# Kernel optimization log

Measured on AMD Instinct MI355X. Metric: run time of the kernel, lower is better.

The kernel has to match this reference:

```python
import jax, jax.numpy as jnp
import numpy as np

EPS = 1e-5


def _bn(h, gamma, beta):
    # BatchNorm1d in training mode: batch statistics over node dim
    mu = h.mean(axis=0)
    var = h.var(axis=0)
    return gamma * (h - mu) * jax.lax.rsqrt(var + EPS) + beta


def _rgcn_layer(x, src, dst, etype, W, Wloop, b, n_dst):
    # Relation-specific gather-transform-scatter (DGL RelGraphConv, sum agg,
    # self-loop + bias, no regularizer).
    x_src = x[src]                                   # [E, in] gather
    num_rels = W.shape[0]
    m = jnp.zeros((x_src.shape[0], W.shape[2]), x.dtype)
    for r in range(num_rels):                        # small fixed relation count
        m = m + jnp.where((etype == r)[:, None], x_src @ W[r], 0.0)
    agg = jax.ops.segment_sum(m, dst, num_segments=n_dst)  # scatter-add to dst
    # DGL block convention: dst nodes are the prefix of src nodes
    return agg + x[:n_dst] @ Wloop + b


def setup_inputs() -> dict:
    key = jax.random.key(0)
    ks = jax.random.split(key, 16)
    N_SRC, N_DST0, N_DST1 = 200000, 50000, 10000
    E0, E1, R, H, C = 800000, 160000, 5, 256, 153
    s = 1.0 / np.sqrt(H)
    inp = {
        "x": jax.random.normal(ks[0], (N_SRC, H), jnp.float32),
        "src0": jax.random.randint(ks[1], (E0,), 0, N_SRC, jnp.int32),
        "dst0": jax.random.randint(ks[2], (E0,), 0, N_DST0, jnp.int32),
        "etype0": jax.random.randint(ks[3], (E0,), 0, R, jnp.int32),
        "src1": jax.random.randint(ks[4], (E1,), 0, N_DST0, jnp.int32),
        "dst1": jax.random.randint(ks[5], (E1,), 0, N_DST1, jnp.int32),
        "etype1": jax.random.randint(ks[6], (E1,), 0, R, jnp.int32),
        "n_dst0": N_DST0,
        "n_dst1": N_DST1,
        "W0": jax.random.normal(ks[7], (R, H, H), jnp.float32) * s,
        "Wl0": jax.random.normal(ks[8], (H, H), jnp.float32) * s,
        "b0": jnp.zeros((H,), jnp.float32),
        "g0": jnp.ones((H,), jnp.float32),
        "be0": jnp.zeros((H,), jnp.float32),
        "W1": jax.random.normal(ks[9], (R, H, H), jnp.float32) * s,
        "Wl1": jax.random.normal(ks[10], (H, H), jnp.float32) * s,
        "b1": jnp.zeros((H,), jnp.float32),
        "g1": jnp.ones((H,), jnp.float32),
        "be1": jnp.zeros((H,), jnp.float32),
        "Wm1": jax.random.normal(ks[11], (H, H), jnp.float32) * s,
        "bm1": jnp.zeros((H,), jnp.float32),
        "gm": jnp.ones((H,), jnp.float32),
        "bem": jnp.zeros((H,), jnp.float32),
        "Wm2": jax.random.normal(ks[12], (H, C), jnp.float32) * s,
        "bm2": jnp.zeros((C,), jnp.float32),
    }
    return inp


def reference(x, src0, dst0, etype0, src1, dst1, etype1, n_dst0, n_dst1,
              W0, Wl0, b0, g0, be0, W1, Wl1, b1, g1, be1,
              Wm1, bm1, gm, bem, Wm2, bm2):
    # layer 0
    h = _rgcn_layer(x, src0, dst0, etype0, W0, Wl0, b0, n_dst0)
    h = jax.nn.elu(_bn(h, g0, be0))
    # layer 1
    h = _rgcn_layer(h, src1, dst1, etype1, W1, Wl1, b1, n_dst1)
    h = jax.nn.elu(_bn(h, g1, be1))
    # MLP head (dropout is identity in eval)
    h = jax.nn.relu(_bn(h @ Wm1 + bm1, gm, bem))
    return h @ Wm2 + bm2
```

## Files before the change

kernel.cpp:

```cpp
#include <hip/hip_runtime.h>
#include <hip/hip_bf16.h>


#define HD   256
#define EPS  1e-5f
#define NREL 5
#define ND0  50000
#define ND1  10000

typedef unsigned short ushort_t;
using f32x4  = __attribute__((ext_vector_type(4))) float;
using short8 = __attribute__((ext_vector_type(8))) short;

__device__ __forceinline__ ushort_t f2b(float f) {
    union { float f; unsigned u; } x; x.f = f;
    unsigned r = x.u + 0x7FFF + ((x.u >> 16) & 1);
    return (ushort_t)(r >> 16);
}
__device__ __forceinline__ float b2f(ushort_t h) {
    union { unsigned u; float f; } x; x.u = ((unsigned)h) << 16;
    return x.f;
}

#define GLOAD_LDS16(gp, lp)                                                     \
    __builtin_amdgcn_global_load_lds(                                           \
        (const __attribute__((address_space(1))) unsigned int*)(gp),            \
        (__attribute__((address_space(3))) unsigned int*)(lp), 16, 0, 0)

struct WconvArgs {
    const float* src[14];
    ushort_t*    dst[14];
    int          N[14];
};
__global__ void wconv_all_kernel(WconvArgs a) {
    int mat = blockIdx.x >> 8;
    int id = (blockIdx.x & 255) * 256 + threadIdx.x;
    int n = id >> 8, k = id & 255;
    int N = a.N[mat];
    float v = (n < N) ? a.src[mat][(size_t)k * N + n] : 0.f;
    a.dst[mat][id] = f2b(v);
}

__global__ void xconv_kernel(const float* __restrict__ x, ushort_t* __restrict__ xb,
                             int n4) {
    int id = blockIdx.x * 256 + threadIdx.x;
    if (id >= n4) return;
    float4 v = ((const float4*)x)[id];
    ushort4 o; o.x = f2b(v.x); o.y = f2b(v.y); o.z = f2b(v.z); o.w = f2b(v.w);
    ((ushort4*)xb)[id] = o;
}

__global__ void count2_kernel(const int* __restrict__ d0, const int* __restrict__ e0, int E0,
                              const int* __restrict__ d1, const int* __restrict__ e1, int E1,
                              int* __restrict__ cnt, int* __restrict__ pos) {
    int e = blockIdx.x * 256 + threadIdx.x;
    if (e < E0) {
        pos[e] = atomicAdd(&cnt[e0[e] * ND0 + d0[e]], 1);
    } else if (e < E0 + E1) {
        int i = e - E0;
        pos[e] = atomicAdd(&cnt[NREL * ND0 + e1[i] * ND1 + d1[i]], 1);
    }
}

__global__ void scan_block_kernel(const int* __restrict__ in, int* __restrict__ out,
                                  int* __restrict__ bsum, int nb) {
    __shared__ int ts[256];
    int tid = threadIdx.x;
    int base = blockIdx.x * 1024 + tid * 4;
    int v0 = (base + 0 < nb) ? in[base + 0] : 0;
    int v1 = (base + 1 < nb) ? in[base + 1] : 0;
    int v2 = (base + 2 < nb) ? in[base + 2] : 0;
    int v3 = (base + 3 < nb) ? in[base + 3] : 0;
    int tsum = v0 + v1 + v2 + v3;
    ts[tid] = tsum;
    __syncthreads();
    for (int d = 1; d < 256; d <<= 1) {
        int t = (tid >= d) ? ts[tid - d] : 0;
        __syncthreads();
        ts[tid] += t;
        __syncthreads();
    }
    int excl = ts[tid] - tsum;
    if (base + 0 < nb) out[base + 0] = excl;
    if (base + 1 < nb) out[base + 1] = excl + v0;
    if (base + 2 < nb) out[base + 2] = excl + v0 + v1;
    if (base + 3 < nb) out[base + 3] = excl + v0 + v1 + v2;
    if (tid == 255 && bsum) bsum[blockIdx.x] = ts[255];
}

__global__ void scan_add_kernel(int* __restrict__ out, const int* __restrict__ bsum, int nb) {
    int i = blockIdx.x * 256 + threadIdx.x;
    if (i < nb) out[i] += bsum[i >> 10];
}

__global__ void fill2_kernel(const int* __restrict__ s0, const int* __restrict__ d0,
                             const int* __restrict__ e0, int E0,
                             const int* __restrict__ s1, const int* __restrict__ d1,
                             const int* __restrict__ e1, int E1,
                             const int* __restrict__ pos, const int* __restrict__ off,
                             int* __restrict__ ssrc) {
    int e = blockIdx.x * 256 + threadIdx.x;
    if (e < E0) {
        ssrc[off[e0[e] * ND0 + d0[e]] + pos[e]] = s0[e];
    } else if (e < E0 + E1) {
        int i = e - E0;
        ssrc[off[NREL * ND0 + e1[i] * ND1 + d1[i]] + pos[e]] = s1[i];
    }
}

__device__ __forceinline__ void bnelu_acc(ushort4 v, const float4& scv, const float4& shv,
                                          float& a0, float& a1, float& a2, float& a3) {
    float f0 = fmaf(b2f(v.x), scv.x, shv.x);
    float f1 = fmaf(b2f(v.y), scv.y, shv.y);
    float f2 = fmaf(b2f(v.z), scv.z, shv.z);
    float f3 = fmaf(b2f(v.w), scv.w, shv.w);
    a0 += f0 > 0.f ? f0 : expm1f(f0);
    a1 += f1 > 0.f ? f1 : expm1f(f1);
    a2 += f2 > 0.f ? f2 : expm1f(f2);
    a3 += f3 > 0.f ? f3 : expm1f(f3);
}

__global__ void gather_kernel(const ushort_t* __restrict__ feat, const int* __restrict__ ssrc,
                              const int* __restrict__ cnt, const int* __restrict__ off,
                              int nbuckets, ushort_t* __restrict__ out,
                              const float* __restrict__ sc, const float* __restrict__ sh) {
    int wave = (blockIdx.x * 256 + threadIdx.x) >> 6;
    int lane = threadIdx.x & 63;
    if (wave >= nbuckets) return;
    int deg = cnt[wave], s = off[wave];
    float a0 = 0, a1 = 0, a2 = 0, a3 = 0;
    if (sc) {
        float4 scv = ((const float4*)sc)[lane];
        float4 shv = ((const float4*)sh)[lane];
        int j = 0;
        for (; j + 4 <= deg; j += 4) {
            int r0 = ssrc[s + j + 0], r1 = ssrc[s + j + 1];
            int r2 = ssrc[s + j + 2], r3 = ssrc[s + j + 3];
            ushort4 v0 = ((const ushort4*)(feat + (size_t)r0 * HD))[lane];
            ushort4 v1 = ((const ushort4*)(feat + (size_t)r1 * HD))[lane];
            ushort4 v2 = ((const ushort4*)(feat + (size_t)r2 * HD))[lane];
            ushort4 v3 = ((const ushort4*)(feat + (size_t)r3 * HD))[lane];
            bnelu_acc(v0, scv, shv, a0, a1, a2, a3);
            bnelu_acc(v1, scv, shv, a0, a1, a2, a3);
            bnelu_acc(v2, scv, shv, a0, a1, a2, a3);
            bnelu_acc(v3, scv, shv, a0, a1, a2, a3);
        }
        for (; j < deg; j++) {
            ushort4 v = ((const ushort4*)(feat + (size_t)ssrc[s + j] * HD))[lane];
            bnelu_acc(v, scv, shv, a0, a1, a2, a3);
        }
    } else {
        int j = 0;
        for (; j + 4 <= deg; j += 4) {
            int r0 = ssrc[s + j + 0], r1 = ssrc[s + j + 1];
            int r2 = ssrc[s + j + 2], r3 = ssrc[s + j + 3];
            ushort4 v0 = ((const ushort4*)(feat + (size_t)r0 * HD))[lane];
            ushort4 v1 = ((const ushort4*)(feat + (size_t)r1 * HD))[lane];
            ushort4 v2 = ((const ushort4*)(feat + (size_t)r2 * HD))[lane];
            ushort4 v3 = ((const ushort4*)(feat + (size_t)r3 * HD))[lane];
            a0 += b2f(v0.x) + b2f(v1.x) + b2f(v2.x) + b2f(v3.x);
            a1 += b2f(v0.y) + b2f(v1.y) + b2f(v2.y) + b2f(v3.y);
            a2 += b2f(v0.z) + b2f(v1.z) + b2f(v2.z) + b2f(v3.z);
            a3 += b2f(v0.w) + b2f(v1.w) + b2f(v2.w) + b2f(v3.w);
        }
        for (; j < deg; j++) {
            ushort4 v = ((const ushort4*)(feat + (size_t)ssrc[s + j] * HD))[lane];
            a0 += b2f(v.x); a1 += b2f(v.y); a2 += b2f(v.z); a3 += b2f(v.w);
        }
    }
    ushort4 o; o.x = f2b(a0); o.y = f2b(a1); o.z = f2b(a2); o.w = f2b(a3);
    ((ushort4*)(out + (size_t)wave * HD))[lane] = o;
}

__global__ void bnprep_kernel(const float* __restrict__ sums, const float* __restrict__ g,
                              const float* __restrict__ be, float invM,
                              float* __restrict__ sc, float* __restrict__ sh) {
    int c = threadIdx.x;
    float mu = sums[c] * invM;
    float var = sums[HD + c] * invM - mu * mu;
    float s = g[c] * rsqrtf(var + EPS);
    sc[c] = s; sh[c] = be[c] - mu * s;
}

struct Seg {
    const ushort_t* A;
    const ushort_t* B;
    const float* sc;
    const float* sh;
    int act;
};
struct GemmArgs {
    Seg seg[6];
    int nseg;
    const float* bias;
    float* stats;
    ushort_t* Cb;
    float* Cf;
    int M, N;
};

template <int BM>
__launch_bounds__(256, 4)
__global__ void gemm_mfma_kernel(GemmArgs g) {
    constexpr int F   = BM / 32;
    constexpr int NFT = BM / 16;
    constexpr int IT  = NFT / 4;
    __shared__ __align__(1024) ushort_t As[2][NFT * 512];
    __shared__ __align__(1024) ushort_t Bs[2][NFT * 512];
    int tid = threadIdx.x;
    int wave = tid >> 6, lane = tid & 63;
    int rq = lane >> 4, ci = lane & 15;
    int wm = (wave >> 1) * (BM / 2), wn = (wave & 1) * (BM / 2);
    int wmf = wm >> 4, wnf = wn >> 4;
    int bm = blockIdx.y * BM, bn = blockIdx.x * BM;
    f32x4 acc[F][F] = {};
    int K = g.nseg * HD;
    int NT = K >> 5;

    auto stage = [&](int b, int t) {
        int k = t << 5;
        int si = k >> 8;
        int kl = k & 255;
        const ushort_t* Ap = g.seg[si].A;
        const ushort_t* Bp = g.seg[si].B;
        const float* sc = g.seg[si].sc;
        if (!sc) {
#pragma unroll
            for (int it = 0; it < IT; it++) {
                int mt = it * 4 + wave;
                GLOAD_LDS16(Ap + (size_t)(bm + mt * 16 + ci) * HD + kl + rq * 8,
                            &As[b][mt * 512 + lane * 8]);
            }
        } else {
            const float* sh = g.seg[si].sh;
            int act = g.seg[si].act;
            int kb = kl + rq * 8;
#pragma unroll
            for (int it = 0; it < IT; it++) {
                int mt = it * 4 + wave;
                uint4 v = *(const uint4*)(Ap + (size_t)(bm + mt * 16 + ci) * HD + kb);
                ushort_t* u = (ushort_t*)&v;
#pragma unroll
                for (int jj = 0; jj < 8; jj++) {
                    float fv = fmaf(b2f(u[jj]), sc[kb + jj], sh[kb + jj]);
                    fv = (act == 2) ? fmaxf(fv, 0.f) : (fv > 0.f ? fv : expm1f(fv));
                    u[jj] = f2b(fv);
                }
                *(uint4*)&As[b][mt * 512 + lane * 8] = v;
            }
        }
#pragma unroll
        for (int it = 0; it < IT; it++) {
            int nt = it * 4 + wave;
            GLOAD_LDS16(Bp + (size_t)(bn + nt * 16 + ci) * HD + kl + rq * 8,
                        &Bs[b][nt * 512 + lane * 8]);
        }
    };

    stage(0, 0);
    __syncthreads();
    for (int t = 0; t < NT; t++) {
        int cur = t & 1;
        if (t + 1 < NT) stage(cur ^ 1, t + 1);
        short8 a[F], b[F];
#pragma unroll
        for (int mi = 0; mi < F; mi++)
            a[mi] = *(const short8*)&As[cur][(wmf + mi) * 512 + lane * 8];
#pragma unroll
        for (int ni = 0; ni < F; ni++)
            b[ni] = *(const short8*)&Bs[cur][(wnf + ni) * 512 + lane * 8];
#pragma unroll
        for (int mi = 0; mi < F; mi++)
#pragma unroll
            for (int ni = 0; ni < F; ni++)
                acc[mi][ni] = __builtin_amdgcn_mfma_f32_16x16x32_bf16(
                    a[mi], b[ni], acc[mi][ni], 0, 0, 0);
        __syncthreads();
    }

#pragma unroll
    for (int ni = 0; ni < F; ni++) {
        int col = bn + wn + ni * 16 + ci;
        float bv = (col < g.N) ? g.bias[col] : 0.f;
#pragma unroll
        for (int mi = 0; mi < F; mi++)
#pragma unroll
            for (int reg = 0; reg < 4; reg++) acc[mi][ni][reg] += bv;
    }
    if (g.stats) {
#pragma unroll
        for (int ni = 0; ni < F; ni++) {
            float s = 0.f, s2 = 0.f;
#pragma unroll
            for (int mi = 0; mi < F; mi++)
#pragma unroll
                for (int reg = 0; reg < 4; reg++) {
                    int row = bm + wm + mi * 16 + rq * 4 + reg;
                    if (row < g.M) { float v = acc[mi][ni][reg]; s += v; s2 += v * v; }
                }
            s  += __shfl_xor(s, 16);  s  += __shfl_xor(s, 32);
            s2 += __shfl_xor(s2, 16); s2 += __shfl_xor(s2, 32);
            if (rq == 0) {
                int col = bn + wn + ni * 16 + ci;
                atomicAdd(&g.stats[col], s);
                atomicAdd(&g.stats[HD + col], s2);
            }
        }
    }
#pragma unroll
    for (int mi = 0; mi < F; mi++)
#pragma unroll
        for (int ni = 0; ni < F; ni++)
#pragma unroll
            for (int reg = 0; reg < 4; reg++) {
                int row = bm + wm + mi * 16 + rq * 4 + reg;
                int col = bn + wn + ni * 16 + ci;
                if (row < g.M && col < g.N) {
                    float v = acc[mi][ni][reg];
                    if (g.Cb) g.Cb[(size_t)row * HD + col] = f2b(v);
                    else      g.Cf[(size_t)row * g.N + col] = v;
                }
            }
}

extern "C" void kernel_launch(void* const* d_in, const int* in_sizes, int n_in,
                              void* d_out, int out_size, void* d_ws, size_t ws_size,
                              hipStream_t stream) {
    const float* x   = (const float*)d_in[0];
    const int* src0  = (const int*)d_in[1];
    const int* dst0  = (const int*)d_in[2];
    const int* et0   = (const int*)d_in[3];
    const int* src1  = (const int*)d_in[4];
    const int* dst1  = (const int*)d_in[5];
    const int* et1   = (const int*)d_in[6];
    const float* W0  = (const float*)d_in[9];
    const float* Wl0 = (const float*)d_in[10];
    const float* b0  = (const float*)d_in[11];
    const float* g0  = (const float*)d_in[12];
    const float* be0 = (const float*)d_in[13];
    const float* W1  = (const float*)d_in[14];
    const float* Wl1 = (const float*)d_in[15];
    const float* b1  = (const float*)d_in[16];
    const float* g1  = (const float*)d_in[17];
    const float* be1 = (const float*)d_in[18];
    const float* Wm1 = (const float*)d_in[19];
    const float* bm1 = (const float*)d_in[20];
    const float* gm  = (const float*)d_in[21];
    const float* bem = (const float*)d_in[22];
    const float* Wm2 = (const float*)d_in[23];
    const float* bm2 = (const float*)d_in[24];

    const int E0 = in_sizes[1];
    const int E1 = in_sizes[4];
    const int NOUT = in_sizes[24];
    const int NSRC = in_sizes[0] / HD;
    const int NBKT = NREL * ND0 + NREL * ND1;

    char* p = (char*)d_ws;
    ushort_t* Wt = (ushort_t*)p;  p += (size_t)14 * 65536 * 2;
    float* st    = (float*)p;     p += 1536 * 4;
    float* bnp   = (float*)p;     p += 6 * 256 * 4;
    int* cnt     = (int*)p;       p += (size_t)NBKT * 4;
    int* off     = (int*)p;       p += (size_t)NBKT * 4;
    int* bsum    = (int*)p;       p += 1024 * 4;
    int* pos     = (int*)p;       p += (size_t)(E0 + E1) * 4;
    int* ssrc    = (int*)p;       p += (size_t)(E0 + E1) * 4;
    ushort_t* xb  = (ushort_t*)p; p += (size_t)NSRC * HD * 2;
    ushort_t* S0  = (ushort_t*)p; p += (size_t)(NREL * ND0 + 128) * HD * 2;
    ushort_t* S1  = (ushort_t*)p; p += (size_t)(NREL * ND1 + 128) * HD * 2;
    ushort_t* h0b = (ushort_t*)p; p += (size_t)(ND0 + 128) * HD * 2;
    ushort_t* h1b = (ushort_t*)p; p += (size_t)(ND1 + 128) * HD * 2;
    ushort_t* mb  = (ushort_t*)p; p += (size_t)(ND1 + 128) * HD * 2;

    float* st0 = st, *st1 = st + 512, *stm = st + 1024;
    float* sc0 = bnp, *sh0 = bnp + 256, *sc1 = bnp + 512, *sh1 = bnp + 768;
    float* scm = bnp + 1024, *shm = bnp + 1280;

    ushort_t* W0t  = Wt;
    ushort_t* Wl0t = Wt + 5 * 65536;
    ushort_t* W1t  = Wt + 6 * 65536;
    ushort_t* Wl1t = Wt + 11 * 65536;
    ushort_t* Wm1t = Wt + 12 * 65536;
    ushort_t* Wm2t = Wt + 13 * 65536;

    {
        WconvArgs wa;
        for (int r = 0; r < NREL; r++) { wa.src[r] = W0 + (size_t)r * 65536; wa.dst[r] = W0t + (size_t)r * 65536; wa.N[r] = 256; }
        wa.src[5] = Wl0; wa.dst[5] = Wl0t; wa.N[5] = 256;
        for (int r = 0; r < NREL; r++) { wa.src[6 + r] = W1 + (size_t)r * 65536; wa.dst[6 + r] = W1t + (size_t)r * 65536; wa.N[6 + r] = 256; }
        wa.src[11] = Wl1; wa.dst[11] = Wl1t; wa.N[11] = 256;
        wa.src[12] = Wm1; wa.dst[12] = Wm1t; wa.N[12] = 256;
        wa.src[13] = Wm2; wa.dst[13] = Wm2t; wa.N[13] = NOUT;
        wconv_all_kernel<<<14 * 256, 256, 0, stream>>>(wa);
    }
    xconv_kernel<<<(NSRC * 64 + 255) / 256, 256, 0, stream>>>(x, xb, NSRC * 64);
    hipMemsetAsync(st, 0, 1536 * sizeof(float), stream);
    hipMemsetAsync(cnt, 0, (size_t)NBKT * sizeof(int), stream);

    int ET = E0 + E1;
    count2_kernel<<<(ET + 255) / 256, 256, 0, stream>>>(dst0, et0, E0, dst1, et1, E1, cnt, pos);
    int nsb = (NBKT + 1023) / 1024;
    scan_block_kernel<<<nsb, 256, 0, stream>>>(cnt, off, bsum, NBKT);
    scan_block_kernel<<<1, 256, 0, stream>>>(bsum, bsum, nullptr, nsb);
    scan_add_kernel<<<(NBKT + 255) / 256, 256, 0, stream>>>(off, bsum, NBKT);
    fill2_kernel<<<(ET + 255) / 256, 256, 0, stream>>>(src0, dst0, et0, E0, src1, dst1, et1, E1, pos, off, ssrc);

    gather_kernel<<<(NREL * ND0 * 64) / 256, 256, 0, stream>>>(
        xb, ssrc, cnt, off, NREL * ND0, S0, nullptr, nullptr);
    {
        GemmArgs ga = {};
        for (int s = 0; s < NREL; s++)
            ga.seg[s] = { S0 + (size_t)s * ND0 * HD, W0t + (size_t)s * 65536, nullptr, nullptr, 0 };
        ga.seg[5] = { xb, Wl0t, nullptr, nullptr, 0 };
        ga.nseg = 6; ga.bias = b0; ga.stats = st0;
        ga.Cb = h0b; ga.Cf = nullptr; ga.M = ND0; ga.N = HD;
        gemm_mfma_kernel<128><<<dim3(2, (ND0 + 127) / 128), 256, 0, stream>>>(ga);
    }
    bnprep_kernel<<<1, 256, 0, stream>>>(st0, g0, be0, 1.f / ND0, sc0, sh0);

    gather_kernel<<<(NREL * ND1 * 64) / 256, 256, 0, stream>>>(
        h0b, ssrc, cnt + NREL * ND0, off + NREL * ND0, NREL * ND1, S1, sc0, sh0);
    {
        GemmArgs ga = {};
        for (int s = 0; s < NREL; s++)
            ga.seg[s] = { S1 + (size_t)s * ND1 * HD, W1t + (size_t)s * 65536, nullptr, nullptr, 0 };
        ga.seg[5] = { h0b, Wl1t, sc0, sh0, 1 };
        ga.nseg = 6; ga.bias = b1; ga.stats = st1;
        ga.Cb = h1b; ga.Cf = nullptr; ga.M = ND1; ga.N = HD;
        gemm_mfma_kernel<64><<<dim3(4, (ND1 + 63) / 64), 256, 0, stream>>>(ga);
    }
    bnprep_kernel<<<1, 256, 0, stream>>>(st1, g1, be1, 1.f / ND1, sc1, sh1);

    {
        GemmArgs ga = {};
        ga.seg[0] = { h1b, Wm1t, sc1, sh1, 1 };
        ga.nseg = 1; ga.bias = bm1; ga.stats = stm;
        ga.Cb = mb; ga.Cf = nullptr; ga.M = ND1; ga.N = HD;
        gemm_mfma_kernel<64><<<dim3(4, (ND1 + 63) / 64), 256, 0, stream>>>(ga);
    }
    bnprep_kernel<<<1, 256, 0, stream>>>(stm, gm, bem, 1.f / ND1, scm, shm);
    {
        GemmArgs ga = {};
        ga.seg[0] = { mb, Wm2t, scm, shm, 2 };
        ga.nseg = 1; ga.bias = bm2; ga.stats = nullptr;
        ga.Cb = nullptr; ga.Cf = (float*)d_out; ga.M = ND1; ga.N = NOUT;
        gemm_mfma_kernel<64><<<dim3((NOUT + 63) / 64, (ND1 + 63) / 64), 256, 0, stream>>>(ga);
    }
}
```

Measured before the change: 774.4 us.

## Use 256x256 tile GEMM with 4-stage pipeline and separate BN-activation pass

Replaces the templated 2-stage GEMM with a single 512-thread kernel that computes a full 256-column tile per block. It uses a 4-deep LDS ring with explicit vmcnt waits and one barrier per k-step. The BN+activation that was fused into the A-operand load is moved into standalone bnact kernels that write activated bf16 copies, so every GEMM can use direct global-to-LDS loads. This trades extra elementwise passes and buffers for larger reuse and deeper prefetch. It also raises LDS use and pushes the 153-column output GEMM through a 256-wide tile.

Result: slower. 808.4 us (+4.4%).

```diff
diff --git a/kernel.cpp b/kernel.cpp
--- a/kernel.cpp
+++ b/kernel.cpp
@@ -182,12 +182,35 @@
     sc[c] = s; sh[c] = be[c] - mu * s;
 }
 
+__global__ void bnact_kernel(const ushort_t* __restrict__ in, ushort_t* __restrict__ out,
+                             const float* __restrict__ sc, const float* __restrict__ sh,
+                             int act, int n64) {
+    int id = blockIdx.x * 256 + threadIdx.x;
+    if (id >= n64) return;
+    int c4 = id & 63;
+    ushort4 v = ((const ushort4*)in)[id];
+    float4 scv = ((const float4*)sc)[c4];
+    float4 shv = ((const float4*)sh)[c4];
+    float f0 = fmaf(b2f(v.x), scv.x, shv.x);
+    float f1 = fmaf(b2f(v.y), scv.y, shv.y);
+    float f2 = fmaf(b2f(v.z), scv.z, shv.z);
+    float f3 = fmaf(b2f(v.w), scv.w, shv.w);
+    if (act == 2) {
+        f0 = fmaxf(f0, 0.f); f1 = fmaxf(f1, 0.f);
+        f2 = fmaxf(f2, 0.f); f3 = fmaxf(f3, 0.f);
+    } else {
+        f0 = f0 > 0.f ? f0 : expm1f(f0);
+        f1 = f1 > 0.f ? f1 : expm1f(f1);
+        f2 = f2 > 0.f ? f2 : expm1f(f2);
+        f3 = f3 > 0.f ? f3 : expm1f(f3);
+    }
+    ushort4 o; o.x = f2b(f0); o.y = f2b(f1); o.z = f2b(f2); o.w = f2b(f3);
+    ((ushort4*)out)[id] = o;
+}
+
 struct Seg {
     const ushort_t* A;
     const ushort_t* B;
-    const float* sc;
-    const float* sh;
-    int act;
 };
 struct GemmArgs {
     Seg seg[6];
@@ -199,100 +222,74 @@
     int M, N;
 };
 
-template <int BM>
-__launch_bounds__(256, 4)
-__global__ void gemm_mfma_kernel(GemmArgs g) {
-    constexpr int F   = BM / 32;
-    constexpr int NFT = BM / 16;
-    constexpr int IT  = NFT / 4;
-    __shared__ __align__(1024) ushort_t As[2][NFT * 512];
-    __shared__ __align__(1024) ushort_t Bs[2][NFT * 512];
+__launch_bounds__(512, 2)
+__global__ void gemm256_kernel(GemmArgs g) {
+    __shared__ __align__(1024) ushort_t As[4][8192];
+    __shared__ __align__(1024) ushort_t Bs[4][8192];
     int tid = threadIdx.x;
-    int wave = tid >> 6, lane = tid & 63;
+    int w = tid >> 6, lane = tid & 63;
     int rq = lane >> 4, ci = lane & 15;
-    int wm = (wave >> 1) * (BM / 2), wn = (wave & 1) * (BM / 2);
-    int wmf = wm >> 4, wnf = wn >> 4;
-    int bm = blockIdx.y * BM, bn = blockIdx.x * BM;
-    f32x4 acc[F][F] = {};
-    int K = g.nseg * HD;
-    int NT = K >> 5;
+    int wm = (w >> 2) * 128, wn = (w & 3) * 64;
+    int bm = blockIdx.y * 256;
+    f32x4 acc[8][4] = {};
+    int NT = (g.nseg * HD) >> 5;
 
     auto stage = [&](int b, int t) {
         int k = t << 5;
-        int si = k >> 8;
-        int kl = k & 255;
+        int si = k >> 8, kl = k & 255;
         const ushort_t* Ap = g.seg[si].A;
         const ushort_t* Bp = g.seg[si].B;
-        const float* sc = g.seg[si].sc;
-        if (!sc) {
-#pragma unroll
-            for (int it = 0; it < IT; it++) {
-                int mt = it * 4 + wave;
-                GLOAD_LDS16(Ap + (size_t)(bm + mt * 16 + ci) * HD + kl + rq * 8,
-                            &As[b][mt * 512 + lane * 8]);
-            }
-        } else {
-            const float* sh = g.seg[si].sh;
-            int act = g.seg[si].act;
-            int kb = kl + rq * 8;
-#pragma unroll
-            for (int it = 0; it < IT; it++) {
-                int mt = it * 4 + wave;
-                uint4 v = *(const uint4*)(Ap + (size_t)(bm + mt * 16 + ci) * HD + kb);
-                ushort_t* u = (ushort_t*)&v;
-#pragma unroll
-                for (int jj = 0; jj < 8; jj++) {
-                    float fv = fmaf(b2f(u[jj]), sc[kb + jj], sh[kb + jj]);
-                    fv = (act == 2) ? fmaxf(fv, 0.f) : (fv > 0.f ? fv : expm1f(fv));
-                    u[jj] = f2b(fv);
-                }
-                *(uint4*)&As[b][mt * 512 + lane * 8] = v;
-            }
-        }
-#pragma unroll
-        for (int it = 0; it < IT; it++) {
-            int nt = it * 4 + wave;
-            GLOAD_LDS16(Bp + (size_t)(bn + nt * 16 + ci) * HD + kl + rq * 8,
-                        &Bs[b][nt * 512 + lane * 8]);
-        }
+        int ft = w * 2;
+        GLOAD_LDS16(Ap + (size_t)(bm + ft * 16 + ci) * HD + kl + rq * 8,
+                    &As[b][ft * 512 + lane * 8]);
+        GLOAD_LDS16(Ap + (size_t)(bm + ft * 16 + 16 + ci) * HD + kl + rq * 8,
+                    &As[b][(ft + 1) * 512 + lane * 8]);
+        GLOAD_LDS16(Bp + (size_t)(ft * 16 + ci) * HD + kl + rq * 8,
+                    &Bs[b][ft * 512 + lane * 8]);
+        GLOAD_LDS16(Bp + (size_t)(ft * 16 + 16 + ci) * HD + kl + rq * 8,
+                    &Bs[b][(ft + 1) * 512 + lane * 8]);
     };
 
     stage(0, 0);
-    __syncthreads();
+    if (NT > 1) stage(1, 1);
+    if (NT > 2) stage(2, 2);
     for (int t = 0; t < NT; t++) {
-        int cur = t & 1;
-        if (t + 1 < NT) stage(cur ^ 1, t + 1);
-        short8 a[F], b[F];
-#pragma unroll
-        for (int mi = 0; mi < F; mi++)
-            a[mi] = *(const short8*)&As[cur][(wmf + mi) * 512 + lane * 8];
-#pragma unroll
-        for (int ni = 0; ni < F; ni++)
-            b[ni] = *(const short8*)&Bs[cur][(wnf + ni) * 512 + lane * 8];
-#pragma unroll
-        for (int mi = 0; mi < F; mi++)
-#pragma unroll
-            for (int ni = 0; ni < F; ni++)
+        int buf = t & 3;
+        int rem = NT - t;
+        if (rem >= 3)      asm volatile("s_waitcnt vmcnt(8)" ::: "memory");
+        else if (rem == 2) asm volatile("s_waitcnt vmcnt(4)" ::: "memory");
+        else               asm volatile("s_waitcnt vmcnt(0)" ::: "memory");
+        __builtin_amdgcn_s_barrier();
+        if (t + 3 < NT) stage((t + 3) & 3, t + 3);
+        short8 bfr[4];
+#pragma unroll
+        for (int ni = 0; ni < 4; ni++)
+            bfr[ni] = *(const short8*)&Bs[buf][((wn >> 4) + ni) * 512 + lane * 8];
+#pragma unroll
+        for (int mi = 0; mi < 8; mi++) {
+            short8 afr = *(const short8*)&As[buf][((wm >> 4) + mi) * 512 + lane * 8];
+#pragma unroll
+            for (int ni = 0; ni < 4; ni++)
                 acc[mi][ni] = __builtin_amdgcn_mfma_f32_16x16x32_bf16(
-                    a[mi], b[ni], acc[mi][ni], 0, 0, 0);
-        __syncthreads();
-    }
-
-#pragma unroll
-    for (int ni = 0; ni < F; ni++) {
-        int col = bn + wn + ni * 16 + ci;
+                    afr, bfr[ni], acc[mi][ni], 0, 0, 0);
+        }
+    }
+
+#pragma unroll
+    for (int ni = 0; ni < 4; ni++) {
+        int col = wn + ni * 16 + ci;
         float bv = (col < g.N) ? g.bias[col] : 0.f;
 #pragma unroll
-        for (int mi = 0; mi < F; mi++)
+        for (int mi = 0; mi < 8; mi++)
 #pragma unroll
             for (int reg = 0; reg < 4; reg++) acc[mi][ni][reg] += bv;
     }
     if (g.stats) {
 #pragma unroll
-        for (int ni = 0; ni < F; ni++) {
+        for (int ni = 0; ni < 4; ni++) {
             float s = 0.f, s2 = 0.f;
 #pragma unroll
-            for (int mi = 0; mi < F; mi++)
+            for (int mi = 0; mi < 8; mi++)
 #pragma unroll
                 for (int reg = 0; reg < 4; reg++) {
                     int row = bm + wm + mi * 16 + rq * 4 + reg;
@@ -301,20 +298,20 @@
             s  += __shfl_xor(s, 16);  s  += __shfl_xor(s, 32);
             s2 += __shfl_xor(s2, 16); s2 += __shfl_xor(s2, 32);
             if (rq == 0) {
-                int col = bn + wn + ni * 16 + ci;
+                int col = wn + ni * 16 + ci;
                 atomicAdd(&g.stats[col], s);
                 atomicAdd(&g.stats[HD + col], s2);
             }
         }
     }
 #pragma unroll
-    for (int mi = 0; mi < F; mi++)
-#pragma unroll
-        for (int ni = 0; ni < F; ni++)
+    for (int mi = 0; mi < 8; mi++)
+#pragma unroll
+        for (int ni = 0; ni < 4; ni++)
 #pragma unroll
             for (int reg = 0; reg < 4; reg++) {
                 int row = bm + wm + mi * 16 + rq * 4 + reg;
-                int col = bn + wn + ni * 16 + ci;
+                int col = wn + ni * 16 + ci;
                 if (row < g.M && col < g.N) {
                     float v = acc[mi][ni][reg];
                     if (g.Cb) g.Cb[(size_t)row * HD + col] = f2b(v);
@@ -366,11 +363,14 @@
     int* pos     = (int*)p;       p += (size_t)(E0 + E1) * 4;
     int* ssrc    = (int*)p;       p += (size_t)(E0 + E1) * 4;
     ushort_t* xb  = (ushort_t*)p; p += (size_t)NSRC * HD * 2;
-    ushort_t* S0  = (ushort_t*)p; p += (size_t)(NREL * ND0 + 128) * HD * 2;
-    ushort_t* S1  = (ushort_t*)p; p += (size_t)(NREL * ND1 + 128) * HD * 2;
-    ushort_t* h0b = (ushort_t*)p; p += (size_t)(ND0 + 128) * HD * 2;
-    ushort_t* h1b = (ushort_t*)p; p += (size_t)(ND1 + 128) * HD * 2;
-    ushort_t* mb  = (ushort_t*)p; p += (size_t)(ND1 + 128) * HD * 2;
+    ushort_t* S0  = (ushort_t*)p; p += (size_t)(NREL * ND0 + 512) * HD * 2;
+    ushort_t* S1  = (ushort_t*)p; p += (size_t)(NREL * ND1 + 512) * HD * 2;
+    ushort_t* h0b = (ushort_t*)p; p += (size_t)(ND0 + 512) * HD * 2;
+    ushort_t* h1b = (ushort_t*)p; p += (size_t)(ND1 + 512) * HD * 2;
+    ushort_t* mb  = (ushort_t*)p; p += (size_t)(ND1 + 512) * HD * 2;
+    ushort_t* h0a = (ushort_t*)p; p += (size_t)(ND1 + 512) * HD * 2;
+    ushort_t* h1a = (ushort_t*)p; p += (size_t)(ND1 + 512) * HD * 2;
+    ushort_t* ma  = (ushort_t*)p; p += (size_t)(ND1 + 512) * HD * 2;
 
     float* st0 = st, *st1 = st + 512, *stm = st + 1024;
     float* sc0 = bnp, *sh0 = bnp + 256, *sc1 = bnp + 512, *sh1 = bnp + 768;
@@ -410,40 +410,46 @@
     {
         GemmArgs ga = {};
         for (int s = 0; s < NREL; s++)
-            ga.seg[s] = { S0 + (size_t)s * ND0 * HD, W0t + (size_t)s * 65536, nullptr, nullptr, 0 };
-        ga.seg[5] = { xb, Wl0t, nullptr, nullptr, 0 };
+            ga.seg[s] = { S0 + (size_t)s * ND0 * HD, W0t + (size_t)s * 65536 };
+        ga.seg[5] = { xb, Wl0t };
         ga.nseg = 6; ga.bias = b0; ga.stats = st0;
         ga.Cb = h0b; ga.Cf = nullptr; ga.M = ND0; ga.N = HD;
-        gemm_mfma_kernel<128><<<dim3(2, (ND0 + 127) / 128), 256, 0, stream>>>(ga);
+        gemm256_kernel<<<dim3(1, (ND0 + 255) / 256), 512, 0, stream>>>(ga);
     }
     bnprep_kernel<<<1, 256, 0, stream>>>(st0, g0, be0, 1.f / ND0, sc0, sh0);
 
+    bnact_kernel<<<((ND1 + 240) * 64 + 255) / 256, 256, 0, stream>>>(
+        h0b, h0a, sc0, sh0, 1, (ND1 + 240) * 64);
     gather_kernel<<<(NREL * ND1 * 64) / 256, 256, 0, stream>>>(
         h0b, ssrc, cnt + NREL * ND0, off + NREL * ND0, NREL * ND1, S1, sc0, sh0);
     {
         GemmArgs ga = {};
         for (int s = 0; s < NREL; s++)
-            ga.seg[s] = { S1 + (size_t)s * ND1 * HD, W1t + (size_t)s * 65536, nullptr, nullptr, 0 };
-        ga.seg[5] = { h0b, Wl1t, sc0, sh0, 1 };
+            ga.seg[s] = { S1 + (size_t)s * ND1 * HD, W1t + (size_t)s * 65536 };
+        ga.seg[5] = { h0a, Wl1t };
         ga.nseg = 6; ga.bias = b1; ga.stats = st1;
         ga.Cb = h1b; ga.Cf = nullptr; ga.M = ND1; ga.N = HD;
-        gemm_mfma_kernel<64><<<dim3(4, (ND1 + 63) / 64), 256, 0, stream>>>(ga);
+        gemm256_kernel<<<dim3(1, (ND1 + 255) / 256), 512, 0, stream>>>(ga);
     }
     bnprep_kernel<<<1, 256, 0, stream>>>(st1, g1, be1, 1.f / ND1, sc1, sh1);
 
+    bnact_kernel<<<((ND1 + 240) * 64 + 255) / 256, 256, 0, stream>>>(
+        h1b, h1a, sc1, sh1, 1, (ND1 + 240) * 64);
     {
         GemmArgs ga = {};
-        ga.seg[0] = { h1b, Wm1t, sc1, sh1, 1 };
+        ga.seg[0] = { h1a, Wm1t };
         ga.nseg = 1; ga.bias = bm1; ga.stats = stm;
         ga.Cb = mb; ga.Cf = nullptr; ga.M = ND1; ga.N = HD;
-        gemm_mfma_kernel<64><<<dim3(4, (ND1 + 63) / 64), 256, 0, stream>>>(ga);
+        gemm256_kernel<<<dim3(1, (ND1 + 255) / 256), 512, 0, stream>>>(ga);
     }
     bnprep_kernel<<<1, 256, 0, stream>>>(stm, gm, bem, 1.f / ND1, scm, shm);
+    bnact_kernel<<<((ND1 + 240) * 64 + 255) / 256, 256, 0, stream>>>(
+        mb, ma, scm, shm, 2, (ND1 + 240) * 64);
     {
         GemmArgs ga = {};
-        ga.seg[0] = { mb, Wm2t, scm, shm, 2 };
+        ga.seg[0] = { ma, Wm2t };
         ga.nseg = 1; ga.bias = bm2; ga.stats = nullptr;
         ga.Cb = nullptr; ga.Cf = (float*)d_out; ga.M = ND1; ga.N = NOUT;
-        gemm_mfma_kernel<64><<<dim3((NOUT + 63) / 64, (ND1 + 63) / 64), 256, 0, stream>>>(ga);
-    }
-}
+        gemm256_kernel<<<dim3(1, (ND1 + 255) / 256), 512, 0, stream>>>(ga);
+    }
+}
```
